# Performance work log

Measured on AMD Instinct MI355X. Metric: run time of the kernel, lower is better.

## Reference

```python
import jax, jax.numpy as jnp
import numpy as np

N_QUBITS = 24          # must be divisible by 3
DIM = 2 ** N_QUBITS    # 16777216 amplitudes
N_GROUPS = N_QUBITS // 3  # 8 disjoint 3-qubit gate applications


def setup_inputs() -> dict:
    key = jax.random.key(0)
    k1, k2, k3 = jax.random.split(key, 3)
    feature = jax.random.normal(k1, (DIM,), dtype=jnp.float32)
    # Build a random 8x8 unitary as expm of an anti-Hermitian generator,
    # mirroring equivar_gate_matrix = expm(generator) in the original.
    m = (jax.random.normal(k2, (8, 8), dtype=jnp.float32)
         + 1j * jax.random.normal(k3, (8, 8), dtype=jnp.float32)).astype(jnp.complex64)
    gen = 0.5 * (m - m.conj().T)
    gate = jax.scipy.linalg.expm(gen)
    return {
        "feature": feature,
        "gate_real": jnp.real(gate).astype(jnp.float32),
        "gate_imag": jnp.imag(gate).astype(jnp.float32),
    }


def _apply_3q_gate(state, gate, axis):
    # state: (8,)*N_GROUPS complex tensor; contract gate (8x8) into `axis`.
    out = jnp.tensordot(gate, state, axes=[[1], [axis]])  # contracted axis -> front
    return jnp.moveaxis(out, 0, axis)


def reference(feature, gate_real, gate_imag):
    # AmplitudeEmbedding: L2-normalize the feature vector into the state.
    norm = jnp.sqrt(jnp.sum(feature * feature))
    state = (feature / norm).astype(jnp.complex64)
    # View the 24 qubits as 8 groups of 3 (each group = one axis of size 8).
    state = state.reshape((8,) * N_GROUPS)
    gate = (gate_real + 1j * gate_imag).astype(jnp.complex64)
    # QubitUnitary(equivar_gate_matrix, wires=(3i, 3i+1, 3i+2)) for each group.
    for g in range(N_GROUPS):
        state = _apply_3q_gate(state, gate, g)
    # qml.probs(): |amplitude|^2 over the full computational basis.
    probs = (jnp.real(state) ** 2 + jnp.imag(state) ** 2).reshape(-1)
    return probs.astype(jnp.float32)
```

## Files before the change

### kernel.cpp

```cpp
#include <hip/hip_runtime.h>


typedef _Float16 f16;
typedef _Float16 f16x4 __attribute__((ext_vector_type(4)));
typedef float f32x4 __attribute__((ext_vector_type(4)));
typedef unsigned int u32;
typedef unsigned short u16;

__device__ __forceinline__ u32 SW1(u32 a) { return a ^ (((a >> 8) & 0xFu) << 3); }
__device__ __forceinline__ u32 SW2(u32 a) { return a ^ (((a >> 7) & 0x7u) << 4); }

__device__ __forceinline__ u32 PK(float x, float y) {
  return __builtin_bit_cast(u32, __builtin_amdgcn_cvt_pkrtz(x, y));
}

__device__ __forceinline__ f16x4 build_A(const float* __restrict__ gr,
                                         const float* __restrict__ gi, int l) {
  const int row = l & 15, kg = l >> 4;
  const int pg = row & 7, rpl = row >> 3, kpl = kg >> 1;
  f16x4 a;
#pragma unroll
  for (int e = 0; e < 4; ++e) {
    const int j = (kg & 1) * 4 + e;
    const float grv = gr[pg * 8 + j], giv = gi[pg * 8 + j];
    const float v = rpl == 0 ? (kpl == 0 ? grv : -giv) : (kpl == 0 ? giv : grv);
    a[e] = (f16)v;
  }
  return a;
}

__device__ __forceinline__ f32x4 MF(f16x4 A, uint2 bw, f32x4 C) {
  return __builtin_amdgcn_mfma_f32_16x16x16f16(A, __builtin_bit_cast(f16x4, bw),
                                               C, 0, 0, 0);
}

template <bool FIRST>
__device__ __forceinline__ void lds_stage(char* lb, f16x4 A, int w, int l) {
  const int kg = l >> 4, c = l & 15, c3 = c >> 3, p = kg >> 1;
  const u32 rb = (u32)(w * 512 + c * 32 + kg * 8);
  const f32x4 Z = {0.f, 0.f, 0.f, 0.f};
  f32x4 acc[16];
#pragma unroll
  for (int g = 0; g < 4; ++g) {
#pragma unroll
    for (int m = 0; m < 4; ++m) {
      const int j = (g & 1) + m * 2 + (g >> 1) * 8;
      uint2 bw = make_uint2(0u, 0u);
      if (!FIRST || kg < 2)
        bw = *(const uint2*)(lb + SW1(rb + (u32)j * 8192u));
      acc[g * 4 + m] = MF(A, bw, Z);
    }
  }
  __syncthreads();
  const u32 wl = (u32)(((w >> 2) << 14) + (((w & 3) * 2 + c3) << 11) +
                       ((c & 7) << 8) + ((kg & 1) << 7) + (p << 4));
#pragma unroll
  for (int g = 0; g < 4; ++g) {
#pragma unroll
    for (int rr = 0; rr < 4; ++rr) {
      const u32 d0 = PK(acc[g * 4 + 0][rr], acc[g * 4 + 1][rr]);
      const u32 d1 = PK(acc[g * 4 + 2][rr], acc[g * 4 + 3][rr]);
      const u32 lg = wl + (u32)(((g & 1) << 16) + ((g >> 1) << 3) + (rr << 5));
      *(uint2*)(lb + SW1(lg)) = make_uint2(d0, d1);
    }
  }
  __syncthreads();
}

__global__ __launch_bounds__(1024, 4) void k_pass1(
    const float* __restrict__ f, const float* __restrict__ gr,
    const float* __restrict__ gi, uint4* __restrict__ st,
    float* __restrict__ wsp) {
  __shared__ __align__(16) char lb[131072];
  __shared__ float red[16];
  const int t = threadIdx.x, l = t & 63, w = t >> 6, blk = blockIdx.x;
  const int kg = l >> 4, c = l & 15, c3 = c >> 3, p = kg >> 1;
  const f16x4 A = build_A(gr, gi, l);
  const f32x4 Z = {0.f, 0.f, 0.f, 0.f};

  float s = 0.f;
  {
    const float4* fin = (const float4*)f + (size_t)blk * 8192;
    float4 vv[8];
#pragma unroll
    for (int d = 0; d < 8; ++d) vv[d] = fin[d * 1024 + t];
#pragma unroll
    for (int d = 0; d < 8; ++d)
      s += vv[d].x * vv[d].x + vv[d].y * vv[d].y + vv[d].z * vv[d].z +
           vv[d].w * vv[d].w;
    const u32 fl = (u32)(((t >> 7) << 14) + (((t >> 4) & 7) << 11) +
                         (((t >> 1) & 7) << 8) + ((t & 1) << 7));
#pragma unroll
    for (int g2 = 0; g2 < 2; ++g2) {
#pragma unroll
      for (int q = 0; q < 4; ++q) {
        const float a0 = q == 0 ? vv[g2 * 4 + 0].x : q == 1 ? vv[g2 * 4 + 0].y
                       : q == 2 ? vv[g2 * 4 + 0].z : vv[g2 * 4 + 0].w;
        const float a1 = q == 0 ? vv[g2 * 4 + 1].x : q == 1 ? vv[g2 * 4 + 1].y
                       : q == 2 ? vv[g2 * 4 + 1].z : vv[g2 * 4 + 1].w;
        const float a2 = q == 0 ? vv[g2 * 4 + 2].x : q == 1 ? vv[g2 * 4 + 2].y
                       : q == 2 ? vv[g2 * 4 + 2].z : vv[g2 * 4 + 2].w;
        const float a3 = q == 0 ? vv[g2 * 4 + 3].x : q == 1 ? vv[g2 * 4 + 3].y
                       : q == 2 ? vv[g2 * 4 + 3].z : vv[g2 * 4 + 3].w;
        const u32 lg = fl + (u32)((q << 5) + (g2 << 3));
        *(uint2*)(lb + SW1(lg)) = make_uint2(PK(a0, a1), PK(a2, a3));
      }
    }
  }
#pragma unroll
  for (int off = 32; off; off >>= 1) s += __shfl_down(s, off, 64);
  if (l == 0) red[w] = s;
  __syncthreads();
  if (t == 0) {
    float a = 0.f;
#pragma unroll
    for (int i = 0; i < 16; ++i) a += red[i];
    wsp[blk] = a;
  }

  lds_stage<true>(lb, A, w, l);
  lds_stage<false>(lb, A, w, l);
  lds_stage<false>(lb, A, w, l);
  lds_stage<false>(lb, A, w, l);

  const u32 rb = (u32)(w * 512 + c * 32 + kg * 8);
  const size_t ob = (size_t)blk * 8192;
#pragma unroll
  for (int j = 0; j < 16; ++j) {
    const uint2 bw = *(const uint2*)(lb + SW1(rb + (u32)j * 8192u));
    const f32x4 a = MF(A, bw, Z);
    const u32 h01 = PK(a[0], a[1]), h23 = PK(a[2], a[3]);
    const u32 q01 = __shfl_xor(h01, 32, 64), q23 = __shfl_xor(h23, 32, 64);
    if (p == 0) {
      const int A3 = j >> 1, A4 = (j & 1) * 4 + (w >> 2), A5 = (w & 3) * 2 + c3;
      uint4 vv;
      vv.x = (h01 & 0xffffu) | (q01 << 16);
      vv.y = (h01 >> 16) | (q01 & 0xffff0000u);
      vv.z = (h23 & 0xffffu) | (q23 << 16);
      vv.w = (h23 >> 16) | (q23 & 0xffff0000u);
      st[ob + (u32)(((A3 * 64 + A4 * 8 + A5) << 4) + ((c & 7) << 1) + (kg & 1))] = vv;
    }
  }
}

__device__ __forceinline__ void p2_stage(char* lb, f16x4 A, int w, int l) {
  const int kg = l >> 4, c = l & 15, pp = kg >> 1;
  const f32x4 Z = {0.f, 0.f, 0.f, 0.f};
  f32x4 acc[16];
#pragma unroll
  for (int g = 0; g < 4; ++g) {
#pragma unroll
    for (int m = 0; m < 4; ++m) {
      const int j = (g & 1) + m * 2 + (g >> 1) * 8;
      const u32 rb = (u32)(j * 2048 + w * 512 + c * 32 + kg * 8);
      const uint2 bw = *(const uint2*)(lb + SW2(rb));
      acc[g * 4 + m] = MF(A, bw, Z);
    }
  }
  __syncthreads();
#pragma unroll
  for (int pe = 0; pe < 2; ++pe) {
#pragma unroll
    for (int rr = 0; rr < 4; ++rr) {
      uint4 vv;
      vv.x = PK(acc[pe * 4 + 0][rr], acc[pe * 4 + 1][rr]);
      vv.y = PK(acc[pe * 4 + 2][rr], acc[pe * 4 + 3][rr]);
      vv.z = PK(acc[(2 + pe) * 4 + 0][rr], acc[(2 + pe) * 4 + 1][rr]);
      vv.w = PK(acc[(2 + pe) * 4 + 2][rr], acc[(2 + pe) * 4 + 3][rr]);
      const u32 wb = (u32)((pe * 4 + w) * 4096 + ((kg & 1) * 4 + rr) * 512 +
                           c * 32 + pp * 16);
      *(uint4*)(lb + SW2(wb)) = vv;
    }
  }
  __syncthreads();
}

__global__ __launch_bounds__(256, 4) void k_pass2(
    const uint4* gp, const float* __restrict__ gr, const float* __restrict__ gi,
    const float* __restrict__ wsp, float* out) {
  __shared__ __align__(16) char lb[32768];
  __shared__ float red[4];
  const int t = threadIdx.x, l = t & 63, w = t >> 6;
  const int kg = l >> 4, c = l & 15, pp = kg >> 1;
  const int b9 = blockIdx.x >> 2, q = blockIdx.x & 3;
  const f16x4 A = build_A(gr, gi, l);
  const f32x4 Z = {0.f, 0.f, 0.f, 0.f};

  float sp_ = wsp[t] + wsp[t + 256];
#pragma unroll
  for (int off = 32; off; off >>= 1) sp_ += __shfl_down(sp_, off, 64);
  if (l == 0) red[w] = sp_;

  {
    const int z = t >> 2, u = t & 3;
    const int A1 = z & 7, A0 = z >> 3;
#pragma unroll
    for (int a2g = 0; a2g < 2; ++a2g) {
      uint4 raw[4];
#pragma unroll
      for (int d = 0; d < 4; ++d)
        raw[d] = gp[(size_t)(z * 8 + 4 * a2g + d) * 8192 + (u32)(b9 * 16 + q * 4 + u)];
#pragma unroll
      for (int v = 0; v < 4; ++v) {
        const u32 w0 = v == 0 ? raw[0].x : v == 1 ? raw[0].y : v == 2 ? raw[0].z : raw[0].w;
        const u32 w1 = v == 0 ? raw[1].x : v == 1 ? raw[1].y : v == 2 ? raw[1].z : raw[1].w;
        const u32 w2 = v == 0 ? raw[2].x : v == 1 ? raw[2].y : v == 2 ? raw[2].z : raw[2].w;
        const u32 w3 = v == 0 ? raw[3].x : v == 1 ? raw[3].y : v == 2 ? raw[3].z : raw[3].w;
        const int sp = u * 4 + v;
        const u32 base = (u32)(A1 * 4096 + A0 * 512 + sp * 32 + 8 * a2g);
        *(uint2*)(lb + SW2(base)) =
            make_uint2((w0 & 0xffffu) | (w1 << 16), (w2 & 0xffffu) | (w3 << 16));
        *(uint2*)(lb + SW2(base + 16u)) =
            make_uint2((w0 >> 16) | (w1 & 0xffff0000u), (w2 >> 16) | (w3 & 0xffff0000u));
      }
    }
  }
  __syncthreads();
  const float inv = 1.0f / (red[0] + red[1] + red[2] + red[3]);

  p2_stage(lb, A, w, l);
  p2_stage(lb, A, w, l);

#pragma unroll
  for (int j = 0; j < 16; ++j) {
    const u32 rb = (u32)(j * 2048 + w * 512 + c * 32 + kg * 8);
    const uint2 bw = *(const uint2*)(lb + SW2(rb));
    const f32x4 a = MF(A, bw, Z);
    const int A2 = j >> 1, A1 = (j & 1) * 4 + w;
    const size_t gb = ((size_t)A1 << 18) + ((size_t)A2 << 15) +
                      (u32)(b9 * 64 + q * 16 + c);
#pragma unroll
    for (int rr = 0; rr < 4; ++rr) {
      float qv = a[rr] * a[rr];
      qv += __shfl_xor(qv, 32, 64);
      if ((rr >> 1) == pp) {
        const size_t A0 = (size_t)((kg & 1) * 4 + rr);
        out[gb + (A0 << 21)] = qv * inv;
      }
    }
  }
}

extern "C" void kernel_launch(void* const* d_in, const int* in_sizes, int n_in,
                              void* d_out, int out_size, void* d_ws,
                              size_t ws_size, hipStream_t stream) {
  (void)in_sizes; (void)n_in; (void)out_size; (void)ws_size;
  const float* f = (const float*)d_in[0];
  const float* gr = (const float*)d_in[1];
  const float* gi = (const float*)d_in[2];
  float* wsp = (float*)d_ws;

  k_pass1<<<dim3(512), dim3(1024), 0, stream>>>(f, gr, gi, (uint4*)d_out, wsp);
  k_pass2<<<dim3(2048), dim3(256), 0, stream>>>((const uint4*)d_out, gr, gi,
                                                wsp, (float*)d_out);
}
```

Measured before the change: 76.85 us.

## Process two tiles per pass-1 block and prefetch second tile during first compute

Pass 1 now launches half as many blocks, each handling two consecutive 8192-float4 tiles. The second tile's global loads are issued into registers before the first tile's LDS/MFMA stages, so memory latency overlaps with compute. A raw barrier separates the first tile's final LDS reads from the second tile's LDS fill. This trades block-level parallelism (256 blocks on a 256-CU device, one wave of 1024-thread blocks) and extra register pressure for explicit software prefetch.

```diff
diff --git a/kernel.cpp b/kernel.cpp
--- a/kernel.cpp
+++ b/kernel.cpp
@@ -13,6 +13,13 @@
 __device__ __forceinline__ u32 PK(float x, float y) {
   return __builtin_bit_cast(u32, __builtin_amdgcn_cvt_pkrtz(x, y));
 }
+
+#define BARRIER_RAW()                                   \
+  do {                                                  \
+    asm volatile("s_waitcnt lgkmcnt(0)" ::: "memory");  \
+    __builtin_amdgcn_sched_barrier(0);                  \
+    __builtin_amdgcn_s_barrier();                       \
+  } while (0)
 
 __device__ __forceinline__ f16x4 build_A(const float* __restrict__ gr,
                                          const float* __restrict__ gi, int l) {
@@ -67,64 +74,43 @@
   __syncthreads();
 }
 
-__global__ __launch_bounds__(1024, 4) void k_pass1(
-    const float* __restrict__ f, const float* __restrict__ gr,
-    const float* __restrict__ gi, uint4* __restrict__ st,
-    float* __restrict__ wsp) {
-  __shared__ __align__(16) char lb[131072];
-  __shared__ float red[16];
-  const int t = threadIdx.x, l = t & 63, w = t >> 6, blk = blockIdx.x;
-  const int kg = l >> 4, c = l & 15, c3 = c >> 3, p = kg >> 1;
-  const f16x4 A = build_A(gr, gi, l);
-  const f32x4 Z = {0.f, 0.f, 0.f, 0.f};
-
+__device__ __forceinline__ float p1_fill(char* lb, const float4* vv, int t) {
   float s = 0.f;
-  {
-    const float4* fin = (const float4*)f + (size_t)blk * 8192;
-    float4 vv[8];
-#pragma unroll
-    for (int d = 0; d < 8; ++d) vv[d] = fin[d * 1024 + t];
-#pragma unroll
-    for (int d = 0; d < 8; ++d)
-      s += vv[d].x * vv[d].x + vv[d].y * vv[d].y + vv[d].z * vv[d].z +
-           vv[d].w * vv[d].w;
-    const u32 fl = (u32)(((t >> 7) << 14) + (((t >> 4) & 7) << 11) +
-                         (((t >> 1) & 7) << 8) + ((t & 1) << 7));
-#pragma unroll
-    for (int g2 = 0; g2 < 2; ++g2) {
-#pragma unroll
-      for (int q = 0; q < 4; ++q) {
-        const float a0 = q == 0 ? vv[g2 * 4 + 0].x : q == 1 ? vv[g2 * 4 + 0].y
-                       : q == 2 ? vv[g2 * 4 + 0].z : vv[g2 * 4 + 0].w;
-        const float a1 = q == 0 ? vv[g2 * 4 + 1].x : q == 1 ? vv[g2 * 4 + 1].y
-                       : q == 2 ? vv[g2 * 4 + 1].z : vv[g2 * 4 + 1].w;
-        const float a2 = q == 0 ? vv[g2 * 4 + 2].x : q == 1 ? vv[g2 * 4 + 2].y
-                       : q == 2 ? vv[g2 * 4 + 2].z : vv[g2 * 4 + 2].w;
-        const float a3 = q == 0 ? vv[g2 * 4 + 3].x : q == 1 ? vv[g2 * 4 + 3].y
-                       : q == 2 ? vv[g2 * 4 + 3].z : vv[g2 * 4 + 3].w;
-        const u32 lg = fl + (u32)((q << 5) + (g2 << 3));
-        *(uint2*)(lb + SW1(lg)) = make_uint2(PK(a0, a1), PK(a2, a3));
-      }
-    }
-  }
-#pragma unroll
-  for (int off = 32; off; off >>= 1) s += __shfl_down(s, off, 64);
-  if (l == 0) red[w] = s;
-  __syncthreads();
-  if (t == 0) {
-    float a = 0.f;
-#pragma unroll
-    for (int i = 0; i < 16; ++i) a += red[i];
-    wsp[blk] = a;
-  }
-
+#pragma unroll
+  for (int d = 0; d < 8; ++d)
+    s += vv[d].x * vv[d].x + vv[d].y * vv[d].y + vv[d].z * vv[d].z +
+         vv[d].w * vv[d].w;
+  const u32 fl = (u32)(((t >> 7) << 14) + (((t >> 4) & 7) << 11) +
+                       (((t >> 1) & 7) << 8) + ((t & 1) << 7));
+#pragma unroll
+  for (int g2 = 0; g2 < 2; ++g2) {
+#pragma unroll
+    for (int q = 0; q < 4; ++q) {
+      const float a0 = q == 0 ? vv[g2 * 4 + 0].x : q == 1 ? vv[g2 * 4 + 0].y
+                     : q == 2 ? vv[g2 * 4 + 0].z : vv[g2 * 4 + 0].w;
+      const float a1 = q == 0 ? vv[g2 * 4 + 1].x : q == 1 ? vv[g2 * 4 + 1].y
+                     : q == 2 ? vv[g2 * 4 + 1].z : vv[g2 * 4 + 1].w;
+      const float a2 = q == 0 ? vv[g2 * 4 + 2].x : q == 1 ? vv[g2 * 4 + 2].y
+                     : q == 2 ? vv[g2 * 4 + 2].z : vv[g2 * 4 + 2].w;
+      const float a3 = q == 0 ? vv[g2 * 4 + 3].x : q == 1 ? vv[g2 * 4 + 3].y
+                     : q == 2 ? vv[g2 * 4 + 3].z : vv[g2 * 4 + 3].w;
+      const u32 lg = fl + (u32)((q << 5) + (g2 << 3));
+      *(uint2*)(lb + SW1(lg)) = make_uint2(PK(a0, a1), PK(a2, a3));
+    }
+  }
+  return s;
+}
+
+__device__ __forceinline__ void p1_tile(char* lb, f16x4 A, int w, int l,
+                                        uint4* __restrict__ st, int tile) {
   lds_stage<true>(lb, A, w, l);
   lds_stage<false>(lb, A, w, l);
   lds_stage<false>(lb, A, w, l);
   lds_stage<false>(lb, A, w, l);
-
+  const int kg = l >> 4, c = l & 15, c3 = c >> 3, p = kg >> 1;
+  const f32x4 Z = {0.f, 0.f, 0.f, 0.f};
   const u32 rb = (u32)(w * 512 + c * 32 + kg * 8);
-  const size_t ob = (size_t)blk * 8192;
+  const size_t ob = (size_t)tile * 8192;
 #pragma unroll
   for (int j = 0; j < 16; ++j) {
     const uint2 bw = *(const uint2*)(lb + SW1(rb + (u32)j * 8192u));
@@ -143,6 +129,54 @@
   }
 }
 
+__global__ __launch_bounds__(1024, 4) void k_pass1(
+    const float* __restrict__ f, const float* __restrict__ gr,
+    const float* __restrict__ gi, uint4* __restrict__ st,
+    float* __restrict__ wsp) {
+  __shared__ __align__(16) char lb[131072];
+  __shared__ float red[16];
+  const int t = threadIdx.x, l = t & 63, w = t >> 6, blk = blockIdx.x;
+  const f16x4 A = build_A(gr, gi, l);
+  const float4* fin = (const float4*)f + (size_t)(2 * blk) * 8192;
+
+  float4 vv[8];
+#pragma unroll
+  for (int d = 0; d < 8; ++d) vv[d] = fin[d * 1024 + t];
+  float s = p1_fill(lb, vv, t);
+#pragma unroll
+  for (int off = 32; off; off >>= 1) s += __shfl_down(s, off, 64);
+  if (l == 0) red[w] = s;
+  __syncthreads();
+  if (t == 0) {
+    float a = 0.f;
+#pragma unroll
+    for (int i = 0; i < 16; ++i) a += red[i];
+    wsp[2 * blk] = a;
+  }
+
+  float4 pv[8];
+#pragma unroll
+  for (int d = 0; d < 8; ++d) pv[d] = fin[8192 + d * 1024 + t];
+
+  p1_tile(lb, A, w, l, st, 2 * blk);
+
+  BARRIER_RAW();
+
+  s = p1_fill(lb, pv, t);
+#pragma unroll
+  for (int off = 32; off; off >>= 1) s += __shfl_down(s, off, 64);
+  if (l == 0) red[w] = s;
+  __syncthreads();
+  if (t == 0) {
+    float a = 0.f;
+#pragma unroll
+    for (int i = 0; i < 16; ++i) a += red[i];
+    wsp[2 * blk + 1] = a;
+  }
+
+  p1_tile(lb, A, w, l, st, 2 * blk + 1);
+}
+
 __device__ __forceinline__ void p2_stage(char* lb, f16x4 A, int w, int l) {
   const int kg = l >> 4, c = l & 15, pp = kg >> 1;
   const f32x4 Z = {0.f, 0.f, 0.f, 0.f};
@@ -250,7 +284,7 @@
   const float* gi = (const float*)d_in[2];
   float* wsp = (float*)d_ws;
 
-  k_pass1<<<dim3(512), dim3(1024), 0, stream>>>(f, gr, gi, (uint4*)d_out, wsp);
+  k_pass1<<<dim3(256), dim3(1024), 0, stream>>>(f, gr, gi, (uint4*)d_out, wsp);
   k_pass2<<<dim3(2048), dim3(256), 0, stream>>>((const uint4*)d_out, gr, gi,
                                                 wsp, (float*)d_out);
 }
```

Measured after the change: 84.16 us. +9.5%, slower.

## Fuse global input load into first MFMA stage and repack pass-1 output stores

Applied to the files above, without the earlier changes.

The first pass no longer stages the fp32 input through LDS. It loads the float4 values directly as MFMA B-operands in the first gate stage, computing the partial norm there and dropping one LDS write/sync round. The final output of pass 1 is also reorganized so every lane (not only half) writes, batching eight j-values into contiguous uint4 stores with a changed state layout. This trades more scattered global loads for removing an LDS round-trip, and the changed output layout must match what pass 2 reads.

```diff
diff --git a/kernel.cpp b/kernel.cpp
--- a/kernel.cpp
+++ b/kernel.cpp
@@ -5,7 +5,6 @@
 typedef _Float16 f16x4 __attribute__((ext_vector_type(4)));
 typedef float f32x4 __attribute__((ext_vector_type(4)));
 typedef unsigned int u32;
-typedef unsigned short u16;
 
 __device__ __forceinline__ u32 SW1(u32 a) { return a ^ (((a >> 8) & 0xFu) << 3); }
 __device__ __forceinline__ u32 SW2(u32 a) { return a ^ (((a >> 7) & 0x7u) << 4); }
@@ -34,24 +33,42 @@
                                                C, 0, 0, 0);
 }
 
-template <bool FIRST>
-__device__ __forceinline__ void lds_stage(char* lb, f16x4 A, int w, int l) {
+template <bool GFIRST>
+__device__ __forceinline__ void p1_stage(char* lb, const float4* fb, f16x4 A,
+                                         int w, int l, float* red) {
   const int kg = l >> 4, c = l & 15, c3 = c >> 3, p = kg >> 1;
   const u32 rb = (u32)(w * 512 + c * 32 + kg * 8);
   const f32x4 Z = {0.f, 0.f, 0.f, 0.f};
   f32x4 acc[16];
+  float s = 0.f;
 #pragma unroll
   for (int g = 0; g < 4; ++g) {
 #pragma unroll
     for (int m = 0; m < 4; ++m) {
       const int j = (g & 1) + m * 2 + (g >> 1) * 8;
       uint2 bw = make_uint2(0u, 0u);
-      if (!FIRST || kg < 2)
+      if (GFIRST) {
+        if (kg < 2) {
+          const int A3 = j >> 1, A4 = (j & 1) * 4 + (w >> 2);
+          const int A5 = (w & 3) * 2 + c3, A6 = c & 7;
+          const int restn = ((A3 * 8 + A4) * 8 + A5) * 8 + A6;
+          const float4 v = fb[restn * 2 + kg];
+          s += v.x * v.x + v.y * v.y + v.z * v.z + v.w * v.w;
+          bw = make_uint2(PK(v.x, v.y), PK(v.z, v.w));
+        }
+      } else {
         bw = *(const uint2*)(lb + SW1(rb + (u32)j * 8192u));
+      }
       acc[g * 4 + m] = MF(A, bw, Z);
     }
   }
-  __syncthreads();
+  if (GFIRST) {
+#pragma unroll
+    for (int off = 32; off; off >>= 1) s += __shfl_down(s, off, 64);
+    if (l == 0) red[w] = s;
+  } else {
+    __syncthreads();
+  }
   const u32 wl = (u32)(((w >> 2) << 14) + (((w & 3) * 2 + c3) << 11) +
                        ((c & 7) << 8) + ((kg & 1) << 7) + (p << 4));
 #pragma unroll
@@ -74,71 +91,51 @@
   __shared__ __align__(16) char lb[131072];
   __shared__ float red[16];
   const int t = threadIdx.x, l = t & 63, w = t >> 6, blk = blockIdx.x;
-  const int kg = l >> 4, c = l & 15, c3 = c >> 3, p = kg >> 1;
+  const int kg = l >> 4, c = l & 15, c3 = c >> 3, p = kg >> 1, kg0 = kg & 1;
   const f16x4 A = build_A(gr, gi, l);
   const f32x4 Z = {0.f, 0.f, 0.f, 0.f};
-
-  float s = 0.f;
-  {
-    const float4* fin = (const float4*)f + (size_t)blk * 8192;
-    float4 vv[8];
-#pragma unroll
-    for (int d = 0; d < 8; ++d) vv[d] = fin[d * 1024 + t];
-#pragma unroll
-    for (int d = 0; d < 8; ++d)
-      s += vv[d].x * vv[d].x + vv[d].y * vv[d].y + vv[d].z * vv[d].z +
-           vv[d].w * vv[d].w;
-    const u32 fl = (u32)(((t >> 7) << 14) + (((t >> 4) & 7) << 11) +
-                         (((t >> 1) & 7) << 8) + ((t & 1) << 7));
-#pragma unroll
-    for (int g2 = 0; g2 < 2; ++g2) {
-#pragma unroll
-      for (int q = 0; q < 4; ++q) {
-        const float a0 = q == 0 ? vv[g2 * 4 + 0].x : q == 1 ? vv[g2 * 4 + 0].y
-                       : q == 2 ? vv[g2 * 4 + 0].z : vv[g2 * 4 + 0].w;
-        const float a1 = q == 0 ? vv[g2 * 4 + 1].x : q == 1 ? vv[g2 * 4 + 1].y
-                       : q == 2 ? vv[g2 * 4 + 1].z : vv[g2 * 4 + 1].w;
-        const float a2 = q == 0 ? vv[g2 * 4 + 2].x : q == 1 ? vv[g2 * 4 + 2].y
-                       : q == 2 ? vv[g2 * 4 + 2].z : vv[g2 * 4 + 2].w;
-        const float a3 = q == 0 ? vv[g2 * 4 + 3].x : q == 1 ? vv[g2 * 4 + 3].y
-                       : q == 2 ? vv[g2 * 4 + 3].z : vv[g2 * 4 + 3].w;
-        const u32 lg = fl + (u32)((q << 5) + (g2 << 3));
-        *(uint2*)(lb + SW1(lg)) = make_uint2(PK(a0, a1), PK(a2, a3));
-      }
-    }
-  }
-#pragma unroll
-  for (int off = 32; off; off >>= 1) s += __shfl_down(s, off, 64);
-  if (l == 0) red[w] = s;
-  __syncthreads();
+  const float4* fb = (const float4*)f + (size_t)blk * 8192;
+
+  p1_stage<true>(lb, fb, A, w, l, red);
   if (t == 0) {
     float a = 0.f;
 #pragma unroll
     for (int i = 0; i < 16; ++i) a += red[i];
     wsp[blk] = a;
   }
-
-  lds_stage<true>(lb, A, w, l);
-  lds_stage<false>(lb, A, w, l);
-  lds_stage<false>(lb, A, w, l);
-  lds_stage<false>(lb, A, w, l);
+  p1_stage<false>(lb, fb, A, w, l, red);
+  p1_stage<false>(lb, fb, A, w, l, red);
+  p1_stage<false>(lb, fb, A, w, l, red);
 
   const u32 rb = (u32)(w * 512 + c * 32 + kg * 8);
   const size_t ob = (size_t)blk * 8192;
-#pragma unroll
-  for (int j = 0; j < 16; ++j) {
-    const uint2 bw = *(const uint2*)(lb + SW1(rb + (u32)j * 8192u));
-    const f32x4 a = MF(A, bw, Z);
-    const u32 h01 = PK(a[0], a[1]), h23 = PK(a[2], a[3]);
-    const u32 q01 = __shfl_xor(h01, 32, 64), q23 = __shfl_xor(h23, 32, 64);
-    if (p == 0) {
-      const int A3 = j >> 1, A4 = (j & 1) * 4 + (w >> 2), A5 = (w & 3) * 2 + c3;
-      uint4 vv;
-      vv.x = (h01 & 0xffffu) | (q01 << 16);
-      vv.y = (h01 >> 16) | (q01 & 0xffff0000u);
-      vv.z = (h23 & 0xffffu) | (q23 << 16);
-      vv.w = (h23 >> 16) | (q23 & 0xffff0000u);
-      st[ob + (u32)(((A3 * 64 + A4 * 8 + A5) << 4) + ((c & 7) << 1) + (kg & 1))] = vv;
+  const int A4v = (w & 3) * 2 + c3, A5v = c & 15 >= 8 ? (c & 7) : (c & 7);
+#pragma unroll
+  for (int jb = 0; jb < 2; ++jb) {
+    u32 arr[2][8];
+#pragma unroll
+    for (int j7 = 0; j7 < 8; ++j7) {
+      const int j = j7 * 2 + jb;
+      const uint2 bw = *(const uint2*)(lb + SW1(rb + (u32)j * 8192u));
+      const f32x4 a = MF(A, bw, Z);
+      const u32 h01 = PK(a[0], a[1]), h23 = PK(a[2], a[3]);
+      const u32 q01 = __shfl_xor(h01, 32, 64), q23 = __shfl_xor(h23, 32, 64);
+      arr[0][j7] = p ? ((q23 & 0xffffu) | (h23 << 16))
+                     : ((h01 & 0xffffu) | (q01 << 16));
+      arr[1][j7] = p ? ((q23 >> 16) | (h23 & 0xffff0000u))
+                     : ((h01 >> 16) | (q01 & 0xffff0000u));
+    }
+    const int A3v = jb * 4 + (w >> 2);
+    const u32 ibase = (u32)(A3v * 1024 + A4v * 128 + A5v * 16);
+#pragma unroll
+    for (int ab = 0; ab < 2; ++ab) {
+      const int A6v = kg0 * 4 + 2 * p + ab;
+#pragma unroll
+      for (int tq = 0; tq < 2; ++tq) {
+        const uint4 vv = make_uint4(arr[ab][4 * tq + 0], arr[ab][4 * tq + 1],
+                                    arr[ab][4 * tq + 2], arr[ab][4 * tq + 3]);
+        st[ob + ibase + (u32)(A6v * 2 + tq)] = vv;
+      }
     }
   }
 }
```

New measurement: 89.63 us. 1.17x slower.
